# Optimization experiments

Measured on AMD Instinct MI355X. Metric: run time of the kernel, lower is better.

The kernel has to match this reference:

```python
import jax, jax.numpy as jnp
import numpy as np


def setup_inputs() -> dict:
    key = jax.random.key(0)
    ks = jax.random.split(key, 8)
    B, S, Ta, D = 64, 512, 8, 768
    return {
        "memory": jax.random.normal(ks[0], (B, S, D), dtype=jnp.float32),
        "aspect_states": jax.random.normal(ks[1], (B, Ta, D), dtype=jnp.float32),
        "input_ids": jnp.ones((B, S), dtype=jnp.int64),
        "input_t_ids": jnp.ones((B, Ta), dtype=jnp.int64),
        "W1": jax.random.normal(ks[2], (3 * D, D), dtype=jnp.float32) * 0.02,
        "b1": jnp.zeros((D,), dtype=jnp.float32),
        "w2": jax.random.normal(ks[3], (D,), dtype=jnp.float32) * 0.02,
        "Wm": jax.random.normal(ks[4], (D, D), dtype=jnp.float32) * 0.02,
        "bm": jnp.zeros((D,), dtype=jnp.float32),
        "Wd": jax.random.normal(ks[5], (D, 3), dtype=jnp.float32) * 0.02,
        "bd": jnp.zeros((3,), dtype=jnp.float32),
    }


def reference(memory, aspect_states, input_ids, input_t_ids, W1, b1, w2, Wm, bm, Wd, bd):
    B, S, D = memory.shape
    memory_len = jnp.sum(input_ids != 0, axis=-1)          # [B]
    aspect_len = jnp.sum(input_t_ids != 0, axis=-1)        # [B]

    # v_a: mean-pooled aspect representation  [B, D]
    v_a = jnp.sum(aspect_states, axis=1) / aspect_len.astype(memory.dtype)[:, None]
    # v_s: mean-pooled sentence representation [B, D]
    v_s = jnp.sum(memory, axis=1) / memory_len.astype(memory.dtype)[:, None]

    # locationed_memory: memory[i, idx] *= 1 - idx/memory_len[i] for idx < memory_len[i]
    idx = jnp.arange(S, dtype=memory.dtype)                 # [S]
    mlen = memory_len.astype(memory.dtype)[:, None]         # [B, 1]
    loc = jnp.where(idx[None, :] < mlen, 1.0 - idx[None, :] / mlen, 1.0)  # [B, S]
    memory = memory * loc[:, :, None]

    # chunked linear1/linear2 scorer, vectorized:
    # c_t = w2 . tanh(W1 @ [m_t ; v_a ; v_s] + b1)
    W1_m, W1_a, W1_s = W1[:D], W1[D:2 * D], W1[2 * D:]
    ctx = v_a @ W1_a + v_s @ W1_s + b1                      # [B, D]
    h = jnp.tanh(jnp.einsum("bsd,de->bse", memory, W1_m) + ctx[:, None, :])
    scores = h @ w2                                         # [B, S]
    alpha = jax.nn.softmax(scores, axis=1)

    v_ts = jnp.einsum("bsd,bs->bd", memory, alpha)          # [B, D]
    v_ns = v_ts + v_s
    v_ms = jnp.tanh(v_ns @ Wm + bm)
    logits = v_ms @ Wd + bd                                 # [B, 3]
    return logits
```

## Files before the change

kernel.cpp:

```cpp
#include <hip/hip_runtime.h>
#include <hip/hip_bf16.h>


#define NB 64
#define NS 512
#define ND 768
#define NTA 8

typedef __attribute__((ext_vector_type(8))) __bf16 bf16x8;
typedef __attribute__((ext_vector_type(4))) float f32x4;

#define OFF_PVS 0u
#define OFF_PVTS 3145728u
#define OFF_PCTX 6291456u
#define OFF_PU 7077888u
#define OFF_PSC 7864320u
#define OFF_VS 9437184u
#define OFF_VA 9633792u
#define OFF_LENS 9830400u
#define OFF_W1MT 9831424u
#define OFF_MP 11011072u

__device__ __forceinline__ float fast_tanh(float x) {
  x = fminf(fmaxf(x, -15.f), 15.f);
  float t = __expf(2.f * x);
  return __fdividef(t - 1.f, t + 1.f);
}

__device__ __forceinline__ unsigned bfpack2(float a, float b) {
  unsigned ua = __float_as_uint(a), ub = __float_as_uint(b);
  ua = (ua + 0x7FFFu + ((ua >> 16) & 1u)) >> 16;
  ub = (ub + 0x7FFFu + ((ub >> 16) & 1u)) >> 16;
  return ua | (ub << 16);
}

__device__ __forceinline__ unsigned short bf16b(float f) {
  unsigned u = __float_as_uint(f);
  u = (u + 0x7FFFu + ((u >> 16) & 1u)) >> 16;
  return (unsigned short)u;
}

__device__ __forceinline__ void async_copy16(const void* g, void* l) {
  __builtin_amdgcn_global_load_lds(
      (const __attribute__((address_space(1))) void*)g,
      (__attribute__((address_space(3))) void*)l, 16, 0, 0);
}

__global__ __launch_bounds__(256) void k_prep_tr(const int* __restrict__ ids,
                                                 const int* __restrict__ tids,
                                                 const float* __restrict__ aspect,
                                                 const float* __restrict__ W1,
                                                 float* __restrict__ v_a,
                                                 float* __restrict__ lens,
                                                 unsigned short* __restrict__ w1mt) {
  int bid = blockIdx.x, tid = threadIdx.x;
  if (bid < 576) {
    __shared__ float tile[32][33];
    int bx = bid % 24, by = bid / 24;
    int tx = tid & 31, ty = tid >> 5;
    for (int j = 0; j < 32; j += 8)
      tile[ty + j][tx] = W1[(size_t)(by * 32 + ty + j) * ND + bx * 32 + tx];
    __syncthreads();
    for (int j = 0; j < 32; j += 8)
      w1mt[(size_t)(bx * 32 + ty + j) * ND + by * 32 + tx] = bf16b(tile[tx][ty + j]);
  } else {
    int b = bid - 576;
    __shared__ int red[256];
    __shared__ float sh_inva;
    int cnt = 0;
    for (int j = tid; j < NS; j += 256) cnt += (ids[b * NS + j] != 0);
    red[tid] = cnt;
    __syncthreads();
    for (int s = 128; s > 0; s >>= 1) {
      if (tid < s) red[tid] += red[tid + s];
      __syncthreads();
    }
    if (tid == 0) {
      int mlen = red[0];
      int acnt = 0;
      for (int t = 0; t < NTA; ++t) acnt += (tids[b * NTA + t] != 0);
      lens[b] = (float)mlen;
      lens[64 + b] = 1.0f / (float)mlen;
      float inva = 1.0f / (float)acnt;
      lens[128 + b] = inva;
      sh_inva = inva;
    }
    __syncthreads();
    float inva = sh_inva;
    for (int j = tid; j < ND; j += 256) {
      float s = 0.f;
      for (int t = 0; t < NTA; ++t) s += aspect[((size_t)b * NTA + t) * ND + j];
      v_a[b * ND + j] = s * inva;
    }
  }
}

__global__ __launch_bounds__(192) void k_vs_mprime(const float* __restrict__ memory,
                                                   const float* __restrict__ lens,
                                                   float* __restrict__ part_vs,
                                                   unsigned short* __restrict__ mp) {
  int sc = blockIdx.x, b = blockIdx.y, tid = threadIdx.x;
  int d0 = tid * 4;
  float inv_mlen = lens[64 + b];
  float mlenf = lens[b];
  float s0 = 0, s1 = 0, s2 = 0, s3 = 0;
#pragma unroll 8
  for (int s = 0; s < 32; ++s) {
    int srow = sc * 32 + s;
    size_t row = (size_t)b * NS + srow;
    const float4 v = *(const float4*)(memory + row * ND + d0);
    s0 += v.x; s1 += v.y; s2 += v.z; s3 += v.w;
    float fs = (float)srow;
    float loc = (fs < mlenf) ? 1.0f - fs * inv_mlen : 1.0f;
    uint2 pk;
    pk.x = bfpack2(v.x * loc, v.y * loc);
    pk.y = bfpack2(v.z * loc, v.w * loc);
    *(uint2*)(mp + row * ND + d0) = pk;
  }
  float4 o;
  o.x = s0 * inv_mlen; o.y = s1 * inv_mlen; o.z = s2 * inv_mlen; o.w = s3 * inv_mlen;
  *(float4*)(part_vs + ((size_t)sc * NB + b) * ND + d0) = o;
}

__global__ __launch_bounds__(192) void k_reduce_vs(const float* __restrict__ part_vs,
                                                   float* __restrict__ v_s) {
  int b = blockIdx.x, tid = threadIdx.x;
  int d0 = tid * 4;
  float a0 = 0, a1 = 0, a2 = 0, a3 = 0;
#pragma unroll
  for (int p = 0; p < 16; ++p) {
    const float4 v = *(const float4*)(part_vs + ((size_t)p * NB + b) * ND + d0);
    a0 += v.x; a1 += v.y; a2 += v.z; a3 += v.w;
  }
  float4 o; o.x = a0; o.y = a1; o.z = a2; o.w = a3;
  *(float4*)(v_s + b * ND + d0) = o;
}

__global__ __launch_bounds__(128) void k_ctx(const float* __restrict__ W1,
                                             const float* __restrict__ v_a,
                                             const float* __restrict__ v_s,
                                             float* __restrict__ ctx_part) {
  int b = blockIdx.x, et = blockIdx.y, dc = blockIdx.z, tid = threadIdx.x;
  __shared__ float vbuf[384];
  for (int j = tid; j < 384; j += 128) {
    int k = dc * 384 + j;
    vbuf[j] = (k < ND) ? v_a[b * ND + k] : v_s[b * ND + (k - ND)];
  }
  __syncthreads();
  int e = et * 128 + tid;
  float acc = 0.f;
  const float* Wk = W1 + (size_t)(ND + dc * 384) * ND + e;
#pragma unroll 8
  for (int j = 0; j < 384; ++j) acc += vbuf[j] * Wk[(size_t)j * ND];
  ctx_part[((size_t)dc * NB + b) * ND + e] = acc;
}

__global__ __launch_bounds__(256) void k_gemm_scores(const unsigned short* __restrict__ mp,
                                                     const unsigned short* __restrict__ w1mt,
                                                     const float* __restrict__ ctx_part,
                                                     const float* __restrict__ b1,
                                                     const float* __restrict__ w2,
                                                     float* __restrict__ sc_part) {
  __shared__ char lds[65536];
  const int tid = threadIdx.x;
  const int wave = tid >> 6, lane = tid & 63;
  const int bid = blockIdx.x;
  const int swz = (bid & 7) * 192 + (bid >> 3);
  const int rt = swz / 6;
  const int et = swz - rt * 6;
  const int row0 = rt * 128, n0 = et * 128;
  const int b = row0 >> 9;
  const int wm = wave & 1, wn = wave >> 1;

  const int lrow = lane >> 3;
  const int qlog = (lane & 7) ^ lrow;
  const char* Abase = (const char*)mp + (size_t)(row0 + lrow) * (ND * 2) + qlog * 16;
  const char* Bbase = (const char*)w1mt + (size_t)(n0 + lrow) * (ND * 2) + qlog * 16;

  f32x4 acc[4][4];
#pragma unroll
  for (int i = 0; i < 4; ++i)
#pragma unroll
    for (int t = 0; t < 4; ++t) acc[i][t] = (f32x4){0.f, 0.f, 0.f, 0.f};

  const int q2 = lane >> 4, c = lane & 15;
  int offA[4][2], offB[4][2];
#pragma unroll
  for (int i = 0; i < 4; ++i) {
    int ml = wm * 64 + i * 16 + c;
    offA[i][0] = ml * 128 + ((q2 ^ (ml & 7)) * 16);
    offA[i][1] = ml * 128 + (((4 + q2) ^ (ml & 7)) * 16);
    int nl = wn * 64 + i * 16 + c;
    offB[i][0] = nl * 128 + ((q2 ^ (nl & 7)) * 16);
    offB[i][1] = nl * 128 + (((4 + q2) ^ (nl & 7)) * 16);
  }

  auto stage = [&](int bufsel, int kb) {
    char* lA = lds + bufsel * 32768;
    char* lB = lA + 16384;
#pragma unroll
    for (int i = 0; i < 4; ++i) {
      int g = wave * 4 + i;
      async_copy16(Abase + (size_t)g * 8 * (ND * 2) + kb, lA + g * 1024);
      async_copy16(Bbase + (size_t)g * 8 * (ND * 2) + kb, lB + g * 1024);
    }
  };

  stage(0, 0);
  __syncthreads();

  int cur = 0;
#pragma unroll 2
  for (int t = 0; t < 12; ++t) {
    if (t < 11) stage(cur ^ 1, (t + 1) * 128);
    const char* lA = lds + cur * 32768;
    const char* lB = lA + 16384;
    bf16x8 af[2][4], bfr[2][4];
#pragma unroll
    for (int kk = 0; kk < 2; ++kk)
#pragma unroll
      for (int i = 0; i < 4; ++i) {
        af[kk][i] = *(const bf16x8*)(lA + offA[i][kk]);
        bfr[kk][i] = *(const bf16x8*)(lB + offB[i][kk]);
      }
#pragma unroll
    for (int kk = 0; kk < 2; ++kk)
#pragma unroll
      for (int i = 0; i < 4; ++i)
#pragma unroll
        for (int t2 = 0; t2 < 4; ++t2)
          acc[i][t2] = __builtin_amdgcn_mfma_f32_16x16x32_bf16(af[kk][i], bfr[kk][t2], acc[i][t2], 0, 0, 0);
    __syncthreads();
    cur ^= 1;
  }

  float ctxv[4], w2v[4];
#pragma unroll
  for (int t = 0; t < 4; ++t) {
    int n = n0 + wn * 64 + t * 16 + c;
    float cx = b1[n];
#pragma unroll
    for (int dc = 0; dc < 4; ++dc) cx += ctx_part[((size_t)dc * NB + b) * ND + n];
    ctxv[t] = cx;
    w2v[t] = w2[n];
  }
  float* scp = sc_part + (size_t)(et * 2 + wn) * (NB * NS);
#pragma unroll
  for (int i = 0; i < 4; ++i) {
#pragma unroll
    for (int r = 0; r < 4; ++r) {
      float s = 0.f;
#pragma unroll
      for (int t = 0; t < 4; ++t) s += fast_tanh(acc[i][t][r] + ctxv[t]) * w2v[t];
      s += __shfl_xor(s, 1, 64);
      s += __shfl_xor(s, 2, 64);
      s += __shfl_xor(s, 4, 64);
      s += __shfl_xor(s, 8, 64);
      if (c == 0) scp[row0 + wm * 64 + i * 16 + q2 * 4 + r] = s;
    }
  }
}

__global__ __launch_bounds__(192) void k_vts(const unsigned short* __restrict__ mp,
                                             const float* __restrict__ sc_part,
                                             float* __restrict__ part_vts) {
  int sc = blockIdx.x, b = blockIdx.y, tid = threadIdx.x;
  int lane = tid & 63, wid = tid >> 6;
  __shared__ float sred[3], sred2[3];
  __shared__ float al[32];
  const float* sp = sc_part + b * NS;
  float v0 = 0, v1 = 0, v2 = 0;
#pragma unroll
  for (int p = 0; p < 12; ++p) {
    const float* spp = sp + (size_t)p * (NB * NS);
    v0 += spp[tid];
    v1 += spp[tid + 192];
    if (tid < 128) v2 += spp[tid + 384];
  }
  if (tid >= 128) v2 = -1e30f;
  float m = fmaxf(fmaxf(v0, v1), v2);
  for (int off = 1; off < 64; off <<= 1) m = fmaxf(m, __shfl_xor(m, off, 64));
  if (lane == 0) sred[wid] = m;
  __syncthreads();
  float M = fmaxf(fmaxf(sred[0], sred[1]), sred[2]);
  float e = __expf(v0 - M) + __expf(v1 - M) + ((tid < 128) ? __expf(v2 - M) : 0.f);
  for (int off = 1; off < 64; off <<= 1) e += __shfl_xor(e, off, 64);
  if (lane == 0) sred2[wid] = e;
  __syncthreads();
  float invS = 1.0f / (sred2[0] + sred2[1] + sred2[2]);
  if (tid < 32) {
    float sv = 0;
#pragma unroll
    for (int p = 0; p < 12; ++p) sv += sp[(size_t)p * (NB * NS) + sc * 32 + tid];
    al[tid] = __expf(sv - M) * invS;
  }
  __syncthreads();

  int d0 = tid * 4;
  float a0 = 0, a1 = 0, a2 = 0, a3 = 0;
#pragma unroll 8
  for (int s = 0; s < 32; ++s) {
    size_t row = (size_t)b * NS + sc * 32 + s;
    uint2 pk = *(const uint2*)(mp + row * ND + d0);
    float a = al[s];
    a0 += a * __uint_as_float(pk.x << 16);
    a1 += a * __uint_as_float(pk.x & 0xFFFF0000u);
    a2 += a * __uint_as_float(pk.y << 16);
    a3 += a * __uint_as_float(pk.y & 0xFFFF0000u);
  }
  float4 o; o.x = a0; o.y = a1; o.z = a2; o.w = a3;
  *(float4*)(part_vts + ((size_t)sc * NB + b) * ND + d0) = o;
}

__global__ __launch_bounds__(128) void k_final1(const float* __restrict__ part_vts,
                                                const float* __restrict__ v_s,
                                                const float* __restrict__ Wm,
                                                float* __restrict__ u_part) {
  int b = blockIdx.x, et = blockIdx.y, dc = blockIdx.z, tid = threadIdx.x;
  __shared__ float vbuf[192];
  for (int j = tid; j < 192; j += 128) {
    int d = dc * 192 + j;
    float v = v_s[b * ND + d];
#pragma unroll
    for (int p = 0; p < 16; ++p) v += part_vts[((size_t)p * NB + b) * ND + d];
    vbuf[j] = v;
  }
  __syncthreads();
  int e = et * 128 + tid;
  float acc = 0.f;
  const float* Wk = Wm + (size_t)(dc * 192) * ND + e;
#pragma unroll 8
  for (int j = 0; j < 192; ++j) acc += vbuf[j] * Wk[(size_t)j * ND];
  u_part[((size_t)dc * NB + b) * ND + e] = acc;
}

__global__ __launch_bounds__(256) void k_final2(const float* __restrict__ u_part,
                                                const float* __restrict__ bm,
                                                const float* __restrict__ Wd,
                                                const float* __restrict__ bd,
                                                float* __restrict__ out) {
  int b = blockIdx.x, tid = threadIdx.x;
  int wid = tid >> 6, lane = tid & 63;
  __shared__ float red[4][3];
  float p0 = 0, p1 = 0, p2 = 0;
  for (int e = tid; e < ND; e += 256) {
    float uv = bm[e];
#pragma unroll
    for (int dc = 0; dc < 4; ++dc) uv += u_part[((size_t)dc * NB + b) * ND + e];
    float vm = fast_tanh(uv);
    p0 += vm * Wd[e * 3 + 0];
    p1 += vm * Wd[e * 3 + 1];
    p2 += vm * Wd[e * 3 + 2];
  }
  for (int off = 1; off < 64; off <<= 1) {
    p0 += __shfl_xor(p0, off, 64);
    p1 += __shfl_xor(p1, off, 64);
    p2 += __shfl_xor(p2, off, 64);
  }
  if (lane == 0) { red[wid][0] = p0; red[wid][1] = p1; red[wid][2] = p2; }
  __syncthreads();
  if (tid == 0) {
    out[b * 3 + 0] = red[0][0] + red[1][0] + red[2][0] + red[3][0] + bd[0];
    out[b * 3 + 1] = red[0][1] + red[1][1] + red[2][1] + red[3][1] + bd[1];
    out[b * 3 + 2] = red[0][2] + red[1][2] + red[2][2] + red[3][2] + bd[2];
  }
}

extern "C" void kernel_launch(void* const* d_in, const int* in_sizes, int n_in,
                              void* d_out, int out_size, void* d_ws, size_t ws_size,
                              hipStream_t stream) {
  const float* memory = (const float*)d_in[0];
  const float* aspect = (const float*)d_in[1];
  const int* ids = (const int*)d_in[2];
  const int* tids = (const int*)d_in[3];
  const float* W1 = (const float*)d_in[4];
  const float* b1 = (const float*)d_in[5];
  const float* w2 = (const float*)d_in[6];
  const float* Wm = (const float*)d_in[7];
  const float* bm = (const float*)d_in[8];
  const float* Wd = (const float*)d_in[9];
  const float* bd = (const float*)d_in[10];
  float* out = (float*)d_out;

  char* ws = (char*)d_ws;
  float* part_vs = (float*)(ws + OFF_PVS);
  float* part_vts = (float*)(ws + OFF_PVTS);
  float* ctx_part = (float*)(ws + OFF_PCTX);
  float* u_part = (float*)(ws + OFF_PU);
  float* sc_part = (float*)(ws + OFF_PSC);
  float* v_s = (float*)(ws + OFF_VS);
  float* v_a = (float*)(ws + OFF_VA);
  float* lens = (float*)(ws + OFF_LENS);
  unsigned short* w1mt = (unsigned short*)(ws + OFF_W1MT);
  unsigned short* mp = (unsigned short*)(ws + OFF_MP);


  k_prep_tr<<<640, 256, 0, stream>>>(ids, tids, aspect, W1, v_a, lens, w1mt);
  k_vs_mprime<<<dim3(16, NB), 192, 0, stream>>>(memory, lens, part_vs, mp);
  k_reduce_vs<<<NB, 192, 0, stream>>>(part_vs, v_s);
  k_ctx<<<dim3(64, 6, 4), 128, 0, stream>>>(W1, v_a, v_s, ctx_part);
  k_gemm_scores<<<1536, 256, 0, stream>>>(mp, w1mt, ctx_part, b1, w2, sc_part);
  k_vts<<<dim3(16, NB), 192, 0, stream>>>(mp, sc_part, part_vts);
  k_final1<<<dim3(64, 6, 4), 128, 0, stream>>>(part_vts, v_s, Wm, u_part);
  k_final2<<<NB, 256, 0, stream>>>(u_part, bm, Wd, bd, out);
}
```

Before: 305.5 us.

## Precompute ctx and softmax once, split v_s pass finer across blocks

Adds a small kernel that reduces the ctx partials plus bias once per batch, so the GEMM epilogue stops summing four partials per column. Adds a dedicated per-batch softmax kernel, so the 16 k_vts blocks no longer each recompute the full 512-score softmax over 12 partials. Also doubles the grid of the v_s/m' pass to 32 chunks of 16 rows for more parallelism, which doubles the partial-sum reduction. The cost is two extra kernel launches and some extra small intermediate buffers.

```diff
diff --git a/kernel.cpp b/kernel.cpp
--- a/kernel.cpp
+++ b/kernel.cpp
@@ -11,15 +11,17 @@
 typedef __attribute__((ext_vector_type(4))) float f32x4;
 
 #define OFF_PVS 0u
-#define OFF_PVTS 3145728u
-#define OFF_PCTX 6291456u
-#define OFF_PU 7077888u
-#define OFF_PSC 7864320u
-#define OFF_VS 9437184u
-#define OFF_VA 9633792u
-#define OFF_LENS 9830400u
-#define OFF_W1MT 9831424u
-#define OFF_MP 11011072u
+#define OFF_PVTS 6291456u
+#define OFF_PCTX 9437184u
+#define OFF_CTX 10223616u
+#define OFF_PU 10420224u
+#define OFF_PSC 11206656u
+#define OFF_ALPHA 12779520u
+#define OFF_VS 12910592u
+#define OFF_VA 13107200u
+#define OFF_LENS 13303808u
+#define OFF_W1MT 13304832u
+#define OFF_MP 14484480u
 
 __device__ __forceinline__ float fast_tanh(float x) {
   x = fminf(fmaxf(x, -15.f), 15.f);
@@ -104,9 +106,9 @@
   float inv_mlen = lens[64 + b];
   float mlenf = lens[b];
   float s0 = 0, s1 = 0, s2 = 0, s3 = 0;
-#pragma unroll 8
-  for (int s = 0; s < 32; ++s) {
-    int srow = sc * 32 + s;
+#pragma unroll
+  for (int s = 0; s < 16; ++s) {
+    int srow = sc * 16 + s;
     size_t row = (size_t)b * NS + srow;
     const float4 v = *(const float4*)(memory + row * ND + d0);
     s0 += v.x; s1 += v.y; s2 += v.z; s3 += v.w;
@@ -128,7 +130,7 @@
   int d0 = tid * 4;
   float a0 = 0, a1 = 0, a2 = 0, a3 = 0;
 #pragma unroll
-  for (int p = 0; p < 16; ++p) {
+  for (int p = 0; p < 32; ++p) {
     const float4 v = *(const float4*)(part_vs + ((size_t)p * NB + b) * ND + d0);
     a0 += v.x; a1 += v.y; a2 += v.z; a3 += v.w;
   }
@@ -155,10 +157,25 @@
   ctx_part[((size_t)dc * NB + b) * ND + e] = acc;
 }
 
+__global__ __launch_bounds__(192) void k_reduce_ctx(const float* __restrict__ ctx_part,
+                                                    const float* __restrict__ b1,
+                                                    float* __restrict__ ctx) {
+  int b = blockIdx.x, tid = threadIdx.x;
+  int d0 = tid * 4;
+  const float4 bb = *(const float4*)(b1 + d0);
+  float a0 = bb.x, a1 = bb.y, a2 = bb.z, a3 = bb.w;
+#pragma unroll
+  for (int p = 0; p < 4; ++p) {
+    const float4 v = *(const float4*)(ctx_part + ((size_t)p * NB + b) * ND + d0);
+    a0 += v.x; a1 += v.y; a2 += v.z; a3 += v.w;
+  }
+  float4 o; o.x = a0; o.y = a1; o.z = a2; o.w = a3;
+  *(float4*)(ctx + b * ND + d0) = o;
+}
+
 __global__ __launch_bounds__(256) void k_gemm_scores(const unsigned short* __restrict__ mp,
                                                      const unsigned short* __restrict__ w1mt,
-                                                     const float* __restrict__ ctx_part,
-                                                     const float* __restrict__ b1,
+                                                     const float* __restrict__ ctx,
                                                      const float* __restrict__ w2,
                                                      float* __restrict__ sc_part) {
   __shared__ char lds[65536];
@@ -238,10 +255,7 @@
 #pragma unroll
   for (int t = 0; t < 4; ++t) {
     int n = n0 + wn * 64 + t * 16 + c;
-    float cx = b1[n];
-#pragma unroll
-    for (int dc = 0; dc < 4; ++dc) cx += ctx_part[((size_t)dc * NB + b) * ND + n];
-    ctxv[t] = cx;
+    ctxv[t] = ctx[b * ND + n];
     w2v[t] = w2[n];
   }
   float* scp = sc_part + (size_t)(et * 2 + wn) * (NB * NS);
@@ -261,41 +275,46 @@
   }
 }
 
+__global__ __launch_bounds__(512) void k_softmax(const float* __restrict__ sc_part,
+                                                 float* __restrict__ alpha) {
+  int b = blockIdx.x, tid = threadIdx.x;
+  int wid = tid >> 6, lane = tid & 63;
+  __shared__ float red[8], red2[8];
+  float v = 0.f;
+#pragma unroll
+  for (int p = 0; p < 12; ++p) v += sc_part[(size_t)p * (NB * NS) + b * NS + tid];
+  float m = v;
+  for (int off = 1; off < 64; off <<= 1) m = fmaxf(m, __shfl_xor(m, off, 64));
+  if (lane == 0) red[wid] = m;
+  __syncthreads();
+  if (tid == 0) {
+    float mm = red[0];
+    for (int i = 1; i < 8; ++i) mm = fmaxf(mm, red[i]);
+    red[0] = mm;
+  }
+  __syncthreads();
+  float M = red[0];
+  float e = __expf(v - M);
+  float s = e;
+  for (int off = 1; off < 64; off <<= 1) s += __shfl_xor(s, off, 64);
+  if (lane == 0) red2[wid] = s;
+  __syncthreads();
+  if (tid == 0) {
+    float ss = 0.f;
+    for (int i = 0; i < 8; ++i) ss += red2[i];
+    red2[0] = ss;
+  }
+  __syncthreads();
+  alpha[b * NS + tid] = e / red2[0];
+}
+
 __global__ __launch_bounds__(192) void k_vts(const unsigned short* __restrict__ mp,
-                                             const float* __restrict__ sc_part,
+                                             const float* __restrict__ alpha,
                                              float* __restrict__ part_vts) {
   int sc = blockIdx.x, b = blockIdx.y, tid = threadIdx.x;
-  int lane = tid & 63, wid = tid >> 6;
-  __shared__ float sred[3], sred2[3];
   __shared__ float al[32];
-  const float* sp = sc_part + b * NS;
-  float v0 = 0, v1 = 0, v2 = 0;
-#pragma unroll
-  for (int p = 0; p < 12; ++p) {
-    const float* spp = sp + (size_t)p * (NB * NS);
-    v0 += spp[tid];
-    v1 += spp[tid + 192];
-    if (tid < 128) v2 += spp[tid + 384];
-  }
-  if (tid >= 128) v2 = -1e30f;
-  float m = fmaxf(fmaxf(v0, v1), v2);
-  for (int off = 1; off < 64; off <<= 1) m = fmaxf(m, __shfl_xor(m, off, 64));
-  if (lane == 0) sred[wid] = m;
-  __syncthreads();
-  float M = fmaxf(fmaxf(sred[0], sred[1]), sred[2]);
-  float e = __expf(v0 - M) + __expf(v1 - M) + ((tid < 128) ? __expf(v2 - M) : 0.f);
-  for (int off = 1; off < 64; off <<= 1) e += __shfl_xor(e, off, 64);
-  if (lane == 0) sred2[wid] = e;
-  __syncthreads();
-  float invS = 1.0f / (sred2[0] + sred2[1] + sred2[2]);
-  if (tid < 32) {
-    float sv = 0;
-#pragma unroll
-    for (int p = 0; p < 12; ++p) sv += sp[(size_t)p * (NB * NS) + sc * 32 + tid];
-    al[tid] = __expf(sv - M) * invS;
-  }
-  __syncthreads();
-
+  if (tid < 32) al[tid] = alpha[b * NS + sc * 32 + tid];
+  __syncthreads();
   int d0 = tid * 4;
   float a0 = 0, a1 = 0, a2 = 0, a3 = 0;
 #pragma unroll 8
@@ -386,8 +405,10 @@
   float* part_vs = (float*)(ws + OFF_PVS);
   float* part_vts = (float*)(ws + OFF_PVTS);
   float* ctx_part = (float*)(ws + OFF_PCTX);
+  float* ctx = (float*)(ws + OFF_CTX);
   float* u_part = (float*)(ws + OFF_PU);
   float* sc_part = (float*)(ws + OFF_PSC);
+  float* alpha = (float*)(ws + OFF_ALPHA);
   float* v_s = (float*)(ws + OFF_VS);
   float* v_a = (float*)(ws + OFF_VA);
   float* lens = (float*)(ws + OFF_LENS);
@@ -396,11 +417,13 @@
 
 
   k_prep_tr<<<640, 256, 0, stream>>>(ids, tids, aspect, W1, v_a, lens, w1mt);
-  k_vs_mprime<<<dim3(16, NB), 192, 0, stream>>>(memory, lens, part_vs, mp);
+  k_vs_mprime<<<dim3(32, NB), 192, 0, stream>>>(memory, lens, part_vs, mp);
   k_reduce_vs<<<NB, 192, 0, stream>>>(part_vs, v_s);
   k_ctx<<<dim3(64, 6, 4), 128, 0, stream>>>(W1, v_a, v_s, ctx_part);
-  k_gemm_scores<<<1536, 256, 0, stream>>>(mp, w1mt, ctx_part, b1, w2, sc_part);
-  k_vts<<<dim3(16, NB), 192, 0, stream>>>(mp, sc_part, part_vts);
+  k_reduce_ctx<<<NB, 192, 0, stream>>>(ctx_part, b1, ctx);
+  k_gemm_scores<<<1536, 256, 0, stream>>>(mp, w1mt, ctx, w2, sc_part);
+  k_softmax<<<NB, 512, 0, stream>>>(sc_part, alpha);
+  k_vts<<<dim3(16, NB), 192, 0, stream>>>(mp, alpha, part_vts);
   k_final1<<<dim3(64, 6, 4), 128, 0, stream>>>(part_vts, v_s, Wm, u_part);
   k_final2<<<NB, 256, 0, stream>>>(u_part, bm, Wd, bd, out);
 }
```

After: 303.3 us, median of 2. Within noise of the previous version (-0.7%).
